# Optimization experiments

Measured on AMD Instinct MI355X. Metric: run time of the kernel, lower is better.

## Reference

```python
import jax, jax.numpy as jnp
import numpy as np

B, D, S, H, A = 32768, 64, 16, 128, 17  # batch, obs_dim, num_skills, hidden, action_dim


def setup_inputs() -> dict:
    key = jax.random.key(0)
    ks = jax.random.split(key, 16)
    n = jax.random.normal
    inp = {
        "obs": n(ks[0], (B, D), dtype=jnp.float32),
        "skill_ids": jax.random.randint(ks[1], (B,), 0, S),
        # per-skill actor MLP params (stacked over skill axis)
        "Wa1": n(ks[2], (S, D, H), dtype=jnp.float32) * (1.0 / np.sqrt(D)),
        "ba1": jnp.zeros((S, H), dtype=jnp.float32),
        "Wa2": n(ks[3], (S, H, H), dtype=jnp.float32) * (1.0 / np.sqrt(H)),
        "ba2": jnp.zeros((S, H), dtype=jnp.float32),
        "Wa3": n(ks[4], (S, H, A), dtype=jnp.float32) * 0.01,
        "ba3": jnp.zeros((S, A), dtype=jnp.float32),
        # per-skill critic MLP params
        "Wc1": n(ks[5], (S, D, H), dtype=jnp.float32) * (1.0 / np.sqrt(D)),
        "bc1": jnp.zeros((S, H), dtype=jnp.float32),
        "Wc2": n(ks[6], (S, H, H), dtype=jnp.float32) * (1.0 / np.sqrt(H)),
        "bc2": jnp.zeros((S, H), dtype=jnp.float32),
        "Wc3": n(ks[7], (S, H, 1), dtype=jnp.float32) * (1.0 / np.sqrt(H)),
        "bc3": jnp.zeros((S, 1), dtype=jnp.float32),
    }
    return inp


def reference(obs, skill_ids, Wa1, ba1, Wa2, ba2, Wa3, ba3, Wc1, bc1, Wc2, bc2, Wc3, bc3):
    act = jnp.tanh
    num_skills = Wa1.shape[0]
    # dense evaluation of ALL skills' actor MLPs (faithful to original)
    ha = act(jnp.einsum('bd,sdh->bsh', obs, Wa1) + ba1)          # [B, S, H]
    ha = act(jnp.einsum('bsh,shk->bsk', ha, Wa2) + ba2)          # [B, S, H]
    logits_all = jnp.einsum('bsh,sha->bsa', ha, Wa3) + ba3       # [B, S, A]
    # dense evaluation of ALL skills' critic MLPs
    hc = act(jnp.einsum('bd,sdh->bsh', obs, Wc1) + bc1)
    hc = act(jnp.einsum('bsh,shk->bsk', hc, Wc2) + bc2)
    values_all = jnp.einsum('bsh,sho->bso', hc, Wc3) + bc3       # [B, S, 1]
    # one-hot gating select (discards S-1 of S computed outputs)
    gate = jax.nn.one_hot(skill_ids, num_skills, dtype=obs.dtype)  # [B, S]
    logits = jnp.sum(logits_all * gate[:, :, None], axis=1)       # [B, A]
    value = jnp.sum(values_all * gate[:, :, None], axis=1).squeeze(-1)  # [B]
    return logits, value
```

## Files before the change

kernel.cpp:

```cpp
#include <hip/hip_runtime.h>

#define Bt 32768
#define Dt 64
#define St 16
#define Ht 128
#define At 17

typedef __attribute__((ext_vector_type(8))) short bf16x8;
typedef __attribute__((ext_vector_type(4))) float f32x4;

#define CNT_OFF   0
#define PERM_OFF  128
#define WB_OFF    1049600
#define OA1 0
#define OA2 16384
#define OA3 49152
#define OC1 57344
#define OC2 73728
#define SKB 106496

__device__ __forceinline__ unsigned short f2bf(float f) {
  union { float f; unsigned u; } v; v.f = f;
  unsigned r = v.u + 0x7FFFu + ((v.u >> 16) & 1u);
  return (unsigned short)(r >> 16);
}

__device__ __forceinline__ unsigned cvtpk(float a, float b) {
  unsigned r;
  asm("v_cvt_pk_bf16_f32 %0, %1, %2" : "=v"(r) : "v"(a), "v"(b));
  return r;
}

__device__ __forceinline__ float tanh_fb(float acc, float b2) {
  const float t = __expf(__builtin_fmaf(acc, 2.0f, b2));
  const float r = __builtin_amdgcn_rcpf(t + 1.0f);
  return __builtin_fmaf(-2.0f, r, 1.0f);
}

__device__ __forceinline__ f32x4 MFMA(bf16x8 a, bf16x8 b, f32x4 c) {
  return __builtin_amdgcn_mfma_f32_16x16x32_bf16(a, b, c, 0, 0, 0);
}

#define LGKM0() asm volatile("s_waitcnt lgkmcnt(0)" ::: "memory")

__device__ __forceinline__ void ldsload16(const char* g, char* l) {
  __builtin_amdgcn_global_load_lds(
      (const __attribute__((address_space(1))) unsigned int*)g,
      (__attribute__((address_space(3))) unsigned int*)l, 16, 0, 0);
}
__device__ __forceinline__ void stageW(const char* g, char* lds, int bytes,
                                       int wave, int lane) {
  for (int c = wave * 1024; c < bytes; c += 4096)
    ldsload16(g + c + lane * 16, lds + c);
}

__global__ __launch_bounds__(256) void k_fused(
    const int* __restrict__ sid, unsigned short* __restrict__ perm,
    int* __restrict__ cnt,
    const float* __restrict__ Wa1, const float* __restrict__ Wa2,
    const float* __restrict__ Wa3, const float* __restrict__ Wc1,
    const float* __restrict__ Wc2, char* __restrict__ G) {
  __shared__ __align__(16) char smem[32768];
  const int tid = threadIdx.x;
  const int bid = blockIdx.x;

  if (bid >= 80) {
    int* lc = (int*)smem;
    int* lb = lc + St;
    const int b = (bid - 80) * 256 + tid;
    if (tid < St) lc[tid] = 0;
    __syncthreads();
    const int s = sid[b];
    const int p = atomicAdd(&lc[s], 1);
    __syncthreads();
    if (tid < St) lb[tid] = atomicAdd(&cnt[tid], lc[tid]);
    __syncthreads();
    perm[s * Bt + lb[s] + p] = (unsigned short)b;
    return;
  }

  const int s = bid / 5, mm = bid % 5;
  char* Gs = G + s * SKB;

  if (mm == 2) {
    const float* src = Wa3 + s * Ht * At;
    for (int e = tid; e < Ht * At; e += 256) {
      const int k = e / At, n = e - k * At;
      *(unsigned short*)(Gs + OA3 + n * 256 + ((2 * k) ^ ((n & 7) << 4))) =
          f2bf(src[e]);
    }
    return;
  }

  const float* src; int K, off;
  if (mm == 0)      { src = Wa1 + s * Dt * Ht; K = 64;  off = OA1; }
  else if (mm == 1) { src = Wa2 + s * Ht * Ht; K = 128; off = OA2; }
  else if (mm == 3) { src = Wc1 + s * Dt * Ht; K = 64;  off = OC1; }
  else              { src = Wc2 + s * Ht * Ht; K = 128; off = OC2; }
  const int SB = 2 * K;
  const int lsb = (K == 128) ? 8 : 7;
  const int pm = (K == 128) ? 15 : 7;

  unsigned short* lds = (unsigned short*)smem;
  for (int it = 0; it < K / 8; ++it) {
    const int f = (it * 256 + tid) * 4;
    const int k = f >> 7, n0 = f & 127;
    const f32x4 v = *(const f32x4*)(src + f);
#pragma unroll
    for (int j = 0; j < 4; ++j) {
      const int n = n0 + j;
      const int byte = n * SB + ((2 * k) ^ (((n >> 2) & pm) << 4));
      lds[byte >> 1] = f2bf(v[j]);
    }
  }
  __syncthreads();
  const int nbytes = 128 * SB;
  for (int it = 0; it < nbytes / 2048; ++it) {
    const int q = (it * 256 + tid) * 8;
    const int n = q >> lsb, r = q & (SB - 1);
    const int srcoff = (r ^ ((n & 7) << 4)) ^ (((n >> 2) & pm) << 4);
    const unsigned long long v8 =
        *(const unsigned long long*)(smem + n * SB + srcoff);
    *(unsigned long long*)(Gs + off + q) = v8;
  }
}

__device__ __forceinline__ bf16x8 wrd(const char* base, int srw, int n, int c,
                                      int lg, int msw) {
  return *(const bf16x8*)(base + n * srw + (((c) + lg * 16) ^ msw));
}

__device__ __forceinline__ void storeh(char* hw, int msw, int lg, int t,
                                       const f32x4 acc, const float* BB) {
  const f32x4 bb = *(const f32x4*)(BB + t * 16 + lg * 4);
  const f32x4 b2 = bb + bb;
  const unsigned lo = cvtpk(tanh_fb(acc[0], b2[0]), tanh_fb(acc[1], b2[1]));
  const unsigned hi = cvtpk(tanh_fb(acc[2], b2[2]), tanh_fb(acc[3], b2[3]));
  *(unsigned long long*)(hw + ((32 * t + 8 * lg) ^ msw)) =
      (unsigned long long)lo | ((unsigned long long)hi << 32);
}

__device__ __forceinline__ void tile_actor(
    int tbase, int rnext, bool dopref, int& rowcur,
    f32x4& cx0, f32x4& cx1, f32x4& cx2, f32x4& cx3,
    const char* wbuf, char* hw, const float* obs,
    const float* ba1s, const float* ba2s, const float* ba3s, float* out,
    int m, int lg, int msw, int wm, int cs) {
  union { bf16x8 v; unsigned u[4]; } XB0, XB1;
  XB0.u[0] = cvtpk(cx0[0], cx0[1]); XB0.u[1] = cvtpk(cx0[2], cx0[3]);
  XB0.u[2] = cvtpk(cx1[0], cx1[1]); XB0.u[3] = cvtpk(cx1[2], cx1[3]);
  XB1.u[0] = cvtpk(cx2[0], cx2[1]); XB1.u[1] = cvtpk(cx2[2], cx2[3]);
  XB1.u[2] = cvtpk(cx3[0], cx3[1]); XB1.u[3] = cvtpk(cx3[2], cx3[3]);
  const int myrow = rowcur;
  if (dopref) {
    const float* ap = obs + rnext * Dt + lg * 8;
    cx0 = *(const f32x4*)(ap);      cx1 = *(const f32x4*)(ap + 4);
    cx2 = *(const f32x4*)(ap + 32); cx3 = *(const f32x4*)(ap + 36);
  }
  rowcur = rnext;
#pragma unroll
  for (int nt = 0; nt < 8; ++nt) {
    const bf16x8 a0 = wrd(wbuf, 128, nt * 16 + m, 0, lg, msw);
    const bf16x8 a1 = wrd(wbuf, 128, nt * 16 + m, 64, lg, msw);
    f32x4 acc = {0.f, 0.f, 0.f, 0.f};
    acc = MFMA(a0, XB0.v, acc);
    acc = MFMA(a1, XB1.v, acc);
    storeh(hw, msw, lg, nt, acc, ba1s);
  }
  LGKM0();
  const bf16x8 h0 = *(const bf16x8*)(hw + ((0   + 16 * lg) ^ msw));
  const bf16x8 h1 = *(const bf16x8*)(hw + ((64  + 16 * lg) ^ msw));
  const bf16x8 h2 = *(const bf16x8*)(hw + ((128 + 16 * lg) ^ msw));
  const bf16x8 h3 = *(const bf16x8*)(hw + ((192 + 16 * lg) ^ msw));
#pragma unroll
  for (int nt = 0; nt < 8; ++nt) {
    const int n = nt * 16 + m;
    const bf16x8 w0 = wrd(wbuf + 16384, 256, n, 0, lg, msw);
    const bf16x8 w1 = wrd(wbuf + 16384, 256, n, 64, lg, msw);
    const bf16x8 w2 = wrd(wbuf + 16384, 256, n, 128, lg, msw);
    const bf16x8 w3 = wrd(wbuf + 16384, 256, n, 192, lg, msw);
    f32x4 acc = {0.f, 0.f, 0.f, 0.f};
    acc = MFMA(w0, h0, acc); acc = MFMA(w1, h1, acc);
    acc = MFMA(w2, h2, acc); acc = MFMA(w3, h3, acc);
    storeh(hw, msw, lg, nt, acc, ba2s);
  }
  LGKM0();
  const bf16x8 H0 = *(const bf16x8*)(hw + ((0   + 16 * lg) ^ msw));
  const bf16x8 H1 = *(const bf16x8*)(hw + ((64  + 16 * lg) ^ msw));
  const bf16x8 H2 = *(const bf16x8*)(hw + ((128 + 16 * lg) ^ msw));
  const bf16x8 H3 = *(const bf16x8*)(hw + ((192 + 16 * lg) ^ msw));
  const char* W3 = wbuf + 49152;
  const bf16x8 e0 = wrd(W3, 256, m, 0, lg, msw);
  const bf16x8 e1 = wrd(W3, 256, m, 64, lg, msw);
  const bf16x8 e2 = wrd(W3, 256, m, 128, lg, msw);
  const bf16x8 e3 = wrd(W3, 256, m, 192, lg, msw);
  const bf16x8 f0 = wrd(W3, 256, 16 + m, 0, lg, msw);
  const bf16x8 f1 = wrd(W3, 256, 16 + m, 64, lg, msw);
  const bf16x8 f2 = wrd(W3, 256, 16 + m, 128, lg, msw);
  const bf16x8 f3 = wrd(W3, 256, 16 + m, 192, lg, msw);
  f32x4 p0 = {0.f, 0.f, 0.f, 0.f}, p1 = {0.f, 0.f, 0.f, 0.f};
  p0 = MFMA(e0, H0, p0); p0 = MFMA(e1, H1, p0);
  p0 = MFMA(e2, H2, p0); p0 = MFMA(e3, H3, p0);
  p1 = MFMA(f0, H0, p1); p1 = MFMA(f1, H1, p1);
  p1 = MFMA(f2, H2, p1); p1 = MFMA(f3, H3, p1);
  if (tbase + wm < cs) {
    float* orow = out + myrow * At;
#pragma unroll
    for (int i = 0; i < 4; ++i)
      orow[4 * lg + i] = p0[i] + ba3s[4 * lg + i];
    if (lg == 0) orow[16] = p1[0] + ba3s[16];
  }
}

__device__ __forceinline__ void tile_critic(
    int tbase, int rnext, bool dopref, int& rowcur,
    f32x4& cx0, f32x4& cx1, f32x4& cx2, f32x4& cx3,
    const char* wbuf, char* hw, const float* obs,
    const float* bc1s, const float* bc2s, const float* wc3s, float bc3s,
    float* out, int m, int lg, int msw, int wm, int cs) {
  union { bf16x8 v; unsigned u[4]; } XB0, XB1;
  XB0.u[0] = cvtpk(cx0[0], cx0[1]); XB0.u[1] = cvtpk(cx0[2], cx0[3]);
  XB0.u[2] = cvtpk(cx1[0], cx1[1]); XB0.u[3] = cvtpk(cx1[2], cx1[3]);
  XB1.u[0] = cvtpk(cx2[0], cx2[1]); XB1.u[1] = cvtpk(cx2[2], cx2[3]);
  XB1.u[2] = cvtpk(cx3[0], cx3[1]); XB1.u[3] = cvtpk(cx3[2], cx3[3]);
  const int myrow = rowcur;
  if (dopref) {
    const float* ap = obs + rnext * Dt + lg * 8;
    cx0 = *(const f32x4*)(ap);      cx1 = *(const f32x4*)(ap + 4);
    cx2 = *(const f32x4*)(ap + 32); cx3 = *(const f32x4*)(ap + 36);
  }
  rowcur = rnext;
#pragma unroll
  for (int nt = 0; nt < 8; ++nt) {
    const bf16x8 a0 = wrd(wbuf, 128, nt * 16 + m, 0, lg, msw);
    const bf16x8 a1 = wrd(wbuf, 128, nt * 16 + m, 64, lg, msw);
    f32x4 acc = {0.f, 0.f, 0.f, 0.f};
    acc = MFMA(a0, XB0.v, acc);
    acc = MFMA(a1, XB1.v, acc);
    storeh(hw, msw, lg, nt, acc, bc1s);
  }
  LGKM0();
  const bf16x8 h0 = *(const bf16x8*)(hw + ((0   + 16 * lg) ^ msw));
  const bf16x8 h1 = *(const bf16x8*)(hw + ((64  + 16 * lg) ^ msw));
  const bf16x8 h2 = *(const bf16x8*)(hw + ((128 + 16 * lg) ^ msw));
  const bf16x8 h3 = *(const bf16x8*)(hw + ((192 + 16 * lg) ^ msw));
  float vp = 0.f;
#pragma unroll
  for (int nt = 0; nt < 8; ++nt) {
    const int n = nt * 16 + m;
    const bf16x8 w0 = wrd(wbuf + 16384, 256, n, 0, lg, msw);
    const bf16x8 w1 = wrd(wbuf + 16384, 256, n, 64, lg, msw);
    const bf16x8 w2 = wrd(wbuf + 16384, 256, n, 128, lg, msw);
    const bf16x8 w3 = wrd(wbuf + 16384, 256, n, 192, lg, msw);
    f32x4 acc = {0.f, 0.f, 0.f, 0.f};
    acc = MFMA(w0, h0, acc); acc = MFMA(w1, h1, acc);
    acc = MFMA(w2, h2, acc); acc = MFMA(w3, h3, acc);
    const f32x4 bb = *(const f32x4*)(bc2s + nt * 16 + lg * 4);
    const f32x4 b2 = bb + bb;
    const f32x4 wv = *(const f32x4*)(wc3s + nt * 16 + lg * 4);
#pragma unroll
    for (int i = 0; i < 4; ++i)
      vp = __builtin_fmaf(tanh_fb(acc[i], b2[i]), wv[i], vp);
  }
  vp += __shfl_xor(vp, 16);
  vp += __shfl_xor(vp, 32);
  if ((m == (threadIdx.x & 63)) && (threadIdx.x & 63) < 16) {
    if (tbase + wm < cs) out[Bt * At + myrow] = vp + bc3s;
  }
}

__global__ __launch_bounds__(256, 2) void k_main(
    const float* __restrict__ obs,
    const float* __restrict__ ba1, const float* __restrict__ ba2,
    const float* __restrict__ ba3, const float* __restrict__ bc1,
    const float* __restrict__ bc2, const float* __restrict__ Wc3,
    const float* __restrict__ bc3,
    const int* __restrict__ cnt, const unsigned short* __restrict__ perm,
    const char* __restrict__ G, float* __restrict__ out) {
  __shared__ __align__(16) char wbuf[57344];
  __shared__ __align__(16) char hbuf[16384];

  const int tid = threadIdx.x;
  const int wave = tid >> 6, lane = tid & 63;
  const int m = lane & 15, lg = lane >> 4;
  const bool actor = (blockIdx.x == 0);
  const int s = blockIdx.y, idx = blockIdx.z;
  const char* Gs = G + s * SKB;
  const int wm = wave * 16 + m;

  const unsigned short* pb = perm + s * Bt;
  int r0 = pb[idx * 64 + wm];
  int r1 = pb[(idx + 16) * 64 + wm];
  int r2 = pb[(idx + 32) * 64 + wm];
  const int cs = cnt[s];

  if (actor) {
    stageW(Gs + OA1, wbuf, 16384, wave, lane);
    stageW(Gs + OA2, wbuf + 16384, 32768, wave, lane);
    stageW(Gs + OA3, wbuf + 49152, 8192, wave, lane);
  } else {
    stageW(Gs + OC1, wbuf, 16384, wave, lane);
    stageW(Gs + OC2, wbuf + 16384, 32768, wave, lane);
  }

  r0 = min(r0, Bt - 1); r1 = min(r1, Bt - 1); r2 = min(r2, Bt - 1);
  const int nt = (cs + 63) >> 6;

  f32x4 cx0, cx1, cx2, cx3;
  {
    const float* ap = obs + r0 * Dt + lg * 8;
    cx0 = *(const f32x4*)(ap);      cx1 = *(const f32x4*)(ap + 4);
    cx2 = *(const f32x4*)(ap + 32); cx3 = *(const f32x4*)(ap + 36);
  }

  char* hw = hbuf + wm * 256;
  const int msw = (m & 7) << 4;
  __syncthreads();

  int rowcur = r0;
  if (actor) {
    const float* ba1s = ba1 + s * Ht;
    const float* ba2s = ba2 + s * Ht;
    const float* ba3s = ba3 + s * At;
    tile_actor(idx * 64, r1, true, rowcur, cx0, cx1, cx2, cx3,
               wbuf, hw, obs, ba1s, ba2s, ba3s, out, m, lg, msw, wm, cs);
    if ((idx + 16) * 64 < cs + 63 && idx + 16 < nt)
      tile_actor((idx + 16) * 64, r2, true, rowcur, cx0, cx1, cx2, cx3,
                 wbuf, hw, obs, ba1s, ba2s, ba3s, out, m, lg, msw, wm, cs);
    if (idx + 32 < nt)
      tile_actor((idx + 32) * 64, r2, false, rowcur, cx0, cx1, cx2, cx3,
                 wbuf, hw, obs, ba1s, ba2s, ba3s, out, m, lg, msw, wm, cs);
  } else {
    const float* bc1s = bc1 + s * Ht;
    const float* bc2s = bc2 + s * Ht;
    const float* wc3s = Wc3 + s * Ht;
    const float bc3s = bc3[s];
    tile_critic(idx * 64, r1, true, rowcur, cx0, cx1, cx2, cx3,
                wbuf, hw, obs, bc1s, bc2s, wc3s, bc3s, out, m, lg, msw, wm, cs);
    if (idx + 16 < nt)
      tile_critic((idx + 16) * 64, r2, true, rowcur, cx0, cx1, cx2, cx3,
                  wbuf, hw, obs, bc1s, bc2s, wc3s, bc3s, out, m, lg, msw, wm, cs);
    if (idx + 32 < nt)
      tile_critic((idx + 32) * 64, r2, false, rowcur, cx0, cx1, cx2, cx3,
                  wbuf, hw, obs, bc1s, bc2s, wc3s, bc3s, out, m, lg, msw, wm, cs);
  }
}

extern "C" void kernel_launch(void* const* d_in, const int* in_sizes, int n_in,
                              void* d_out, int out_size, void* d_ws, size_t ws_size,
                              hipStream_t stream) {
  const float* obs = (const float*)d_in[0];
  const int* sid   = (const int*)d_in[1];
  const float* Wa1 = (const float*)d_in[2];
  const float* ba1 = (const float*)d_in[3];
  const float* Wa2 = (const float*)d_in[4];
  const float* ba2 = (const float*)d_in[5];
  const float* Wa3 = (const float*)d_in[6];
  const float* ba3 = (const float*)d_in[7];
  const float* Wc1 = (const float*)d_in[8];
  const float* bc1 = (const float*)d_in[9];
  const float* Wc2 = (const float*)d_in[10];
  const float* bc2 = (const float*)d_in[11];
  const float* Wc3 = (const float*)d_in[12];
  const float* bc3 = (const float*)d_in[13];
  float* out = (float*)d_out;
  char* ws = (char*)d_ws;

  int* cnt = (int*)(ws + CNT_OFF);
  unsigned short* perm = (unsigned short*)(ws + PERM_OFF);
  char* G = ws + WB_OFF;

  hipMemsetAsync(cnt, 0, St * sizeof(int), stream);
  k_fused<<<dim3(208), dim3(256), 0, stream>>>(sid, perm, cnt, Wa1, Wa2, Wa3, Wc1, Wc2, G);
  k_main<<<dim3(2, 16, 16), dim3(256), 0, stream>>>(
      obs, ba1, ba2, ba3, bc1, bc2, Wc3, bc3, cnt, perm, G, out);
}
```

Before: 27.83 us.

## Use ballot-based counting sort and split large weight conversion across blocks

The skill-bucketing phase now uses 16 blocks that each handle 2048 rows. Each wave counts skills with ballot/popcount, one global atomic per skill per block reserves space, and rows are scattered with rank-within-wave offsets. This replaces the 128 blocks that did a per-element LDS atomic each. The conversion of the 128x128 weight matrices to bf16 is split into two column halves, so each prep block does half the work, with 7 blocks per skill. A redundant condition in the actor tile guard and in the critic output lane check is also simplified. Bucket ordering stays deterministic within a block but each block now loops over 16 skills with ballots.

Result: slower. 34.07 us (+22.4%).

```diff
diff --git a/kernel.cpp b/kernel.cpp
--- a/kernel.cpp
+++ b/kernel.cpp
@@ -64,25 +64,59 @@
   const int tid = threadIdx.x;
   const int bid = blockIdx.x;
 
-  if (bid >= 80) {
-    int* lc = (int*)smem;
-    int* lb = lc + St;
-    const int b = (bid - 80) * 256 + tid;
-    if (tid < St) lc[tid] = 0;
+  if (bid >= 112) {
+    __shared__ int wh[4][16], wbs[4][16];
+    const int b = bid - 112;
+    const int w = tid >> 6, lane = tid & 63;
+    const int ebase = b * 2048 + w * 512;
+    int c[16];
+#pragma unroll
+    for (int sk = 0; sk < 16; ++sk) c[sk] = 0;
+#pragma unroll
+    for (int r = 0; r < 8; ++r) {
+      const int v = sid[ebase + r * 64 + lane];
+#pragma unroll
+      for (int sk = 0; sk < 16; ++sk)
+        c[sk] += (int)__popcll(__ballot(v == sk));
+    }
+    if (lane == 0) {
+#pragma unroll
+      for (int sk = 0; sk < 16; ++sk) wh[w][sk] = c[sk];
+    }
     __syncthreads();
-    const int s = sid[b];
-    const int p = atomicAdd(&lc[s], 1);
+    if (tid < 16) {
+      const int sk = tid;
+      const int t0 = wh[0][sk], t1 = wh[1][sk], t2 = wh[2][sk], t3 = wh[3][sk];
+      const int g = atomicAdd(&cnt[sk], t0 + t1 + t2 + t3);
+      wbs[0][sk] = g;
+      wbs[1][sk] = g + t0;
+      wbs[2][sk] = g + t0 + t1;
+      wbs[3][sk] = g + t0 + t1 + t2;
+    }
     __syncthreads();
-    if (tid < St) lb[tid] = atomicAdd(&cnt[tid], lc[tid]);
-    __syncthreads();
-    perm[s * Bt + lb[s] + p] = (unsigned short)b;
+    int wb[16];
+#pragma unroll
+    for (int sk = 0; sk < 16; ++sk) wb[sk] = wbs[w][sk];
+    const unsigned long long lt = (1ULL << lane) - 1ULL;
+#pragma unroll
+    for (int r = 0; r < 8; ++r) {
+      const int e = ebase + r * 64 + lane;
+      const int v = sid[e];
+#pragma unroll
+      for (int sk = 0; sk < 16; ++sk) {
+        const unsigned long long mk = __ballot(v == sk);
+        if (v == sk) perm[sk * Bt + wb[sk] + (int)__popcll(mk & lt)] =
+            (unsigned short)e;
+        wb[sk] += (int)__popcll(mk);
+      }
+    }
     return;
   }
 
-  const int s = bid / 5, mm = bid % 5;
+  const int s = bid / 7, t = bid % 7;
   char* Gs = G + s * SKB;
 
-  if (mm == 2) {
+  if (t == 3) {
     const float* src = Wa3 + s * Ht * At;
     for (int e = tid; e < Ht * At; e += 256) {
       const int k = e / At, n = e - k * At;
@@ -92,36 +126,53 @@
     return;
   }
 
-  const float* src; int K, off;
-  if (mm == 0)      { src = Wa1 + s * Dt * Ht; K = 64;  off = OA1; }
-  else if (mm == 1) { src = Wa2 + s * Ht * Ht; K = 128; off = OA2; }
-  else if (mm == 3) { src = Wc1 + s * Dt * Ht; K = 64;  off = OC1; }
-  else              { src = Wc2 + s * Ht * Ht; K = 128; off = OC2; }
-  const int SB = 2 * K;
-  const int lsb = (K == 128) ? 8 : 7;
-  const int pm = (K == 128) ? 15 : 7;
-
   unsigned short* lds = (unsigned short*)smem;
-  for (int it = 0; it < K / 8; ++it) {
-    const int f = (it * 256 + tid) * 4;
-    const int k = f >> 7, n0 = f & 127;
-    const f32x4 v = *(const f32x4*)(src + f);
-#pragma unroll
-    for (int j = 0; j < 4; ++j) {
-      const int n = n0 + j;
-      const int byte = n * SB + ((2 * k) ^ (((n >> 2) & pm) << 4));
-      lds[byte >> 1] = f2bf(v[j]);
-    }
-  }
-  __syncthreads();
-  const int nbytes = 128 * SB;
-  for (int it = 0; it < nbytes / 2048; ++it) {
-    const int q = (it * 256 + tid) * 8;
-    const int n = q >> lsb, r = q & (SB - 1);
-    const int srcoff = (r ^ ((n & 7) << 4)) ^ (((n >> 2) & pm) << 4);
-    const unsigned long long v8 =
-        *(const unsigned long long*)(smem + n * SB + srcoff);
-    *(unsigned long long*)(Gs + off + q) = v8;
+  if (t == 0 || t == 4) {
+    const float* src = (t == 0 ? Wa1 : Wc1) + s * Dt * Ht;
+    const int off = (t == 0) ? OA1 : OC1;
+    for (int it = 0; it < 8; ++it) {
+      const int f = (it * 256 + tid) * 4;
+      const int k = f >> 7, n0 = f & 127;
+      const f32x4 v = *(const f32x4*)(src + f);
+#pragma unroll
+      for (int j = 0; j < 4; ++j) {
+        const int n = n0 + j;
+        const int byte = n * 128 + ((2 * k) ^ (((n >> 2) & 7) << 4));
+        lds[byte >> 1] = f2bf(v[j]);
+      }
+    }
+    __syncthreads();
+    for (int it = 0; it < 8; ++it) {
+      const int q = (it * 256 + tid) * 8;
+      const int n = q >> 7, r = q & 127;
+      const int srcoff = (r ^ ((n & 7) << 4)) ^ (((n >> 2) & 7) << 4);
+      *(unsigned long long*)(Gs + off + q) =
+          *(const unsigned long long*)(smem + n * 128 + srcoff);
+    }
+  } else {
+    const bool isA = (t <= 2);
+    const float* src = (isA ? Wa2 : Wc2) + s * Ht * Ht;
+    const int off = isA ? OA2 : OC2;
+    const int nhalf = ((t == 2) || (t == 6)) ? 64 : 0;
+    for (int it = 0; it < 8; ++it) {
+      const int e4 = it * 256 + tid;
+      const int k = e4 >> 4, nl0 = (e4 & 15) * 4;
+      const f32x4 v = *(const f32x4*)(src + k * 128 + nhalf + nl0);
+#pragma unroll
+      for (int j = 0; j < 4; ++j) {
+        const int nl = nl0 + j;
+        const int byte = nl * 256 + ((2 * k) ^ (((nl >> 2) & 15) << 4));
+        lds[byte >> 1] = f2bf(v[j]);
+      }
+    }
+    __syncthreads();
+    for (int it = 0; it < 8; ++it) {
+      const int q = (it * 256 + tid) * 8;
+      const int nl = q >> 8, r = q & 255;
+      const int srcoff = (r ^ ((nl & 7) << 4)) ^ (((nl >> 2) & 15) << 4);
+      *(unsigned long long*)(Gs + off + (nhalf + nl) * 256 + r) =
+          *(const unsigned long long*)(smem + nl * 256 + srcoff);
+    }
   }
 }
 
@@ -217,7 +268,7 @@
     f32x4& cx0, f32x4& cx1, f32x4& cx2, f32x4& cx3,
     const char* wbuf, char* hw, const float* obs,
     const float* bc1s, const float* bc2s, const float* wc3s, float bc3s,
-    float* out, int m, int lg, int msw, int wm, int cs) {
+    float* out, int m, int lg, int msw, int wm, int cs, int lane) {
   union { bf16x8 v; unsigned u[4]; } XB0, XB1;
   XB0.u[0] = cvtpk(cx0[0], cx0[1]); XB0.u[1] = cvtpk(cx0[2], cx0[3]);
   XB0.u[2] = cvtpk(cx1[0], cx1[1]); XB0.u[3] = cvtpk(cx1[2], cx1[3]);
@@ -264,9 +315,7 @@
   }
   vp += __shfl_xor(vp, 16);
   vp += __shfl_xor(vp, 32);
-  if ((m == (threadIdx.x & 63)) && (threadIdx.x & 63) < 16) {
-    if (tbase + wm < cs) out[Bt * At + myrow] = vp + bc3s;
-  }
+  if (lane < 16 && (tbase + wm < cs)) out[Bt * At + myrow] = vp + bc3s;
 }
 
 __global__ __launch_bounds__(256, 2) void k_main(
@@ -324,7 +373,7 @@
     const float* ba3s = ba3 + s * At;
     tile_actor(idx * 64, r1, true, rowcur, cx0, cx1, cx2, cx3,
                wbuf, hw, obs, ba1s, ba2s, ba3s, out, m, lg, msw, wm, cs);
-    if ((idx + 16) * 64 < cs + 63 && idx + 16 < nt)
+    if (idx + 16 < nt)
       tile_actor((idx + 16) * 64, r2, true, rowcur, cx0, cx1, cx2, cx3,
                  wbuf, hw, obs, ba1s, ba2s, ba3s, out, m, lg, msw, wm, cs);
     if (idx + 32 < nt)
@@ -336,13 +385,13 @@
     const float* wc3s = Wc3 + s * Ht;
     const float bc3s = bc3[s];
     tile_critic(idx * 64, r1, true, rowcur, cx0, cx1, cx2, cx3,
-                wbuf, hw, obs, bc1s, bc2s, wc3s, bc3s, out, m, lg, msw, wm, cs);
+                wbuf, hw, obs, bc1s, bc2s, wc3s, bc3s, out, m, lg, msw, wm, cs, lane);
     if (idx + 16 < nt)
       tile_critic((idx + 16) * 64, r2, true, rowcur, cx0, cx1, cx2, cx3,
-                  wbuf, hw, obs, bc1s, bc2s, wc3s, bc3s, out, m, lg, msw, wm, cs);
+                  wbuf, hw, obs, bc1s, bc2s, wc3s, bc3s, out, m, lg, msw, wm, cs, lane);
     if (idx + 32 < nt)
       tile_critic((idx + 32) * 64, r2, false, rowcur, cx0, cx1, cx2, cx3,
-                  wbuf, hw, obs, bc1s, bc2s, wc3s, bc3s, out, m, lg, msw, wm, cs);
+                  wbuf, hw, obs, bc1s, bc2s, wc3s, bc3s, out, m, lg, msw, wm, cs, lane);
   }
 }
 
@@ -371,7 +420,7 @@
   char* G = ws + WB_OFF;
 
   hipMemsetAsync(cnt, 0, St * sizeof(int), stream);
-  k_fused<<<dim3(208), dim3(256), 0, stream>>>(sid, perm, cnt, Wa1, Wa2, Wa3, Wc1, Wc2, G);
+  k_fused<<<dim3(128), dim3(256), 0, stream>>>(sid, perm, cnt, Wa1, Wa2, Wa3, Wc1, Wc2, G);
   k_main<<<dim3(2, 16, 16), dim3(256), 0, stream>>>(
       obs, ba1, ba2, ba3, bc1, bc2, Wc3, bc3, cnt, perm, G, out);
 }
```
